# Kernel tuning notes

Hardware: AMD Instinct MI355X
Metric: run time of the kernel (lower is better)

## Reference

```python
import jax, jax.numpy as jnp
import numpy as np

N_EMBD = 1024
NUM_HEADS = 16
HEAD_DIM = N_EMBD // NUM_HEADS
B, N = 4, 1024
EPS = 1e-5


def _ln(x, w, b):
    mu = jnp.mean(x, axis=-1, keepdims=True)
    var = jnp.var(x, axis=-1, keepdims=True)
    return (x - mu) * jax.lax.rsqrt(var + EPS) * w + b


def setup_inputs() -> dict:
    key = jax.random.key(0)
    ks = jax.random.split(key, 12)
    s = 0.02
    d, dff = N_EMBD, 4 * N_EMBD
    return {
        "x": jax.random.normal(ks[0], (B, N, d), dtype=jnp.float32),
        "ln1_w": jnp.ones((d,), jnp.float32),
        "ln1_b": jnp.zeros((d,), jnp.float32),
        "Wq": jax.random.normal(ks[1], (d, d), jnp.float32) * s,
        "bq": jnp.zeros((d,), jnp.float32),
        "Wk": jax.random.normal(ks[2], (d, d), jnp.float32) * s,
        "bk": jnp.zeros((d,), jnp.float32),
        "Wv": jax.random.normal(ks[3], (d, d), jnp.float32) * s,
        "bv": jnp.zeros((d,), jnp.float32),
        "Wo": jax.random.normal(ks[4], (d, d), jnp.float32) * s,
        "bo": jnp.zeros((d,), jnp.float32),
        "ln2_w": jnp.ones((d,), jnp.float32),
        "ln2_b": jnp.zeros((d,), jnp.float32),
        "Wfc": jax.random.normal(ks[5], (d, dff), jnp.float32) * s,
        "bfc": jnp.zeros((dff,), jnp.float32),
        "Wproj": jax.random.normal(ks[6], (dff, d), jnp.float32) * s,
        "bproj": jnp.zeros((d,), jnp.float32),
    }


def reference(x, ln1_w, ln1_b, Wq, bq, Wk, bk, Wv, bv, Wo, bo,
              ln2_w, ln2_b, Wfc, bfc, Wproj, bproj):
    # --- attention sublayer ---
    h = _ln(x, ln1_w, ln1_b)  # [B,N,D]
    q = (h @ Wq + bq).reshape(B, N, NUM_HEADS, HEAD_DIM).transpose(0, 2, 1, 3)
    k = (h @ Wk + bk).reshape(B, N, NUM_HEADS, HEAD_DIM).transpose(0, 2, 1, 3)
    v = (h @ Wv + bv).reshape(B, N, NUM_HEADS, HEAD_DIM).transpose(0, 2, 1, 3)
    scale = 1.0 / np.sqrt(HEAD_DIM).astype(np.float32)
    attn = jax.nn.softmax(jnp.einsum("bhqd,bhkd->bhqk", q, k) * scale, axis=-1)
    o = jnp.einsum("bhqk,bhkd->bhqd", attn, v)  # [B,H,N,Dh]
    o = o.transpose(0, 2, 1, 3).reshape(B, N, N_EMBD)
    x = x + (o @ Wo + bo)
    # --- MLP sublayer (exact GELU, matching torch nn.GELU default) ---
    h2 = _ln(x, ln2_w, ln2_b)
    h2 = jax.nn.gelu(h2 @ Wfc + bfc, approximate=False)
    x = x + (h2 @ Wproj + bproj)
    return x
```

## Files before the change

### kernel.cpp

```cpp
#include <hip/hip_runtime.h>
#include <hip/hip_bf16.h>

typedef unsigned short u16;
typedef u16 u16x8 __attribute__((ext_vector_type(8)));
typedef u16 u16x4 __attribute__((ext_vector_type(4)));
typedef __bf16 bf16x8 __attribute__((ext_vector_type(8)));
typedef float f32x4 __attribute__((ext_vector_type(4)));

__device__ __forceinline__ u16 f2bf(float f) {
  union { __hip_bfloat16 h; u16 u; } cv;
  cv.h = __float2bfloat16(f);
  return cv.u;
}
__device__ __forceinline__ float bf2f(u16 u) {
  union { unsigned u; float f; } c;
  c.u = ((unsigned)u) << 16;
  return c.f;
}

__device__ __forceinline__ void glds16(const void* g, void* l) {
  __builtin_amdgcn_global_load_lds(
      (const __attribute__((address_space(1))) unsigned int*)g,
      (__attribute__((address_space(3))) unsigned int*)l, 16, 0, 0);
}

__global__ __launch_bounds__(256) void transpose_bf16(const float* __restrict__ W,
                                                      u16* __restrict__ Wt,
                                                      int K, int N) {
  __shared__ float tile[32][33];
  int tx = threadIdx.x, ty = threadIdx.y;
  int n0 = blockIdx.x * 32, k0 = blockIdx.y * 32;
#pragma unroll
  for (int j = 0; j < 4; ++j)
    tile[ty + j * 8][tx] = W[(size_t)(k0 + ty + j * 8) * N + n0 + tx];
  __syncthreads();
#pragma unroll
  for (int j = 0; j < 4; ++j)
    Wt[(size_t)(n0 + ty + j * 8) * K + k0 + tx] = f2bf(tile[tx][ty + j * 8]);
}

__global__ __launch_bounds__(256) void ln_kernel(const float* __restrict__ x,
                                                 const float* __restrict__ w,
                                                 const float* __restrict__ b,
                                                 u16* __restrict__ out) {
  int row = blockIdx.x, t = threadIdx.x;
  const float* xr = x + (size_t)row * 1024;
  float4 v = *reinterpret_cast<const float4*>(xr + t * 4);
  float s = v.x + v.y + v.z + v.w;
  float s2 = v.x * v.x + v.y * v.y + v.z * v.z + v.w * v.w;
#pragma unroll
  for (int m = 1; m < 64; m <<= 1) {
    s += __shfl_xor(s, m, 64);
    s2 += __shfl_xor(s2, m, 64);
  }
  __shared__ float red[8];
  if ((t & 63) == 0) { red[t >> 6] = s; red[(t >> 6) + 4] = s2; }
  __syncthreads();
  s = red[0] + red[1] + red[2] + red[3];
  s2 = red[4] + red[5] + red[6] + red[7];
  float mu = s * (1.f / 1024.f);
  float var = s2 * (1.f / 1024.f) - mu * mu;
  float rs = rsqrtf(var + 1e-5f);
  float4 wv = *reinterpret_cast<const float4*>(w + t * 4);
  float4 bv = *reinterpret_cast<const float4*>(b + t * 4);
  u16x4 o;
  o.x = f2bf((v.x - mu) * rs * wv.x + bv.x);
  o.y = f2bf((v.y - mu) * rs * wv.y + bv.y);
  o.z = f2bf((v.z - mu) * rs * wv.z + bv.z);
  o.w = f2bf((v.w - mu) * rs * wv.w + bv.w);
  *reinterpret_cast<u16x4*>(out + (size_t)row * 1024 + t * 4) = o;
}

template <int MODE>
__global__ __launch_bounds__(512, 2) void gemm256(
    const u16* __restrict__ A, const u16* __restrict__ Bt,
    const float* __restrict__ b0, const float* __restrict__ b1,
    const float* __restrict__ b2,
    u16* __restrict__ o0, u16* __restrict__ o1, u16* __restrict__ o2,
    int Kfull, int KL, int MT, int NT, float qscale) {
  __shared__ u16 lds[2][2][2][256 * 32];
  const int tid = threadIdx.x;
  const int lane = tid & 63, w = tid >> 6;
  const int wm = w >> 2, wn = w & 3;
  const int l15 = lane & 15, l4 = lane >> 4;
  const int skey = (l15 >> 1) & 3;

  const int nwg = gridDim.x;
  int wg = (int)blockIdx.x;
  wg = (wg & 7) * (nwg >> 3) + (wg >> 3);
  const int mt = wg % MT;
  int rest = wg / MT;
  const int nt = rest % NT;
  const int zt = rest / NT;

  const int row0 = mt * 256, col0 = nt * 256;
  const int kbase = zt * KL;
  const int nkt = KL >> 6;

  auto stage = [&](int buf, int op, int ks, int kt) {
    const u16* src = op ? Bt : A;
    const int base = op ? col0 : row0;
    const int kb = kbase + (kt << 6) + (ks << 5);
    u16* dst = &lds[buf][op][ks][0];
#pragma unroll
    for (int i = 0; i < 2; ++i) {
      int c = i * 512 + tid;
      int r = c >> 2, ch = c & 3;
      int sch = ch ^ ((r >> 1) & 3);
      glds16(src + (size_t)(base + r) * Kfull + kb + sch * 8, dst + c * 8);
    }
  };
  auto rdA = [&](int buf, int ks, int m) -> bf16x8 {
    int row = wm * 128 + m * 16 + l15;
    return *reinterpret_cast<const bf16x8*>(&lds[buf][0][ks][row * 32 + ((l4 ^ skey) << 3)]);
  };
  auto rdB = [&](int buf, int ks, int n) -> bf16x8 {
    int row = wn * 64 + n * 16 + l15;
    return *reinterpret_cast<const bf16x8*>(&lds[buf][1][ks][row * 32 + ((l4 ^ skey) << 3)]);
  };

  f32x4 acc[8][4];
#pragma unroll
  for (int m = 0; m < 8; ++m)
#pragma unroll
    for (int n = 0; n < 4; ++n) acc[m][n] = (f32x4){0.f, 0.f, 0.f, 0.f};

  stage(0, 0, 0, 0);
  stage(0, 0, 1, 0);
  stage(0, 1, 0, 0);
  stage(0, 1, 1, 0);
  asm volatile("s_waitcnt vmcnt(2)" ::: "memory");
  __builtin_amdgcn_s_barrier();

  bf16x8 af[8];
  for (int t = 0; t < nkt; ++t) {
    const int cur = t & 1, nxt = cur ^ 1;
    const bool pf = (t + 1 < nkt);
    {
#pragma unroll
      for (int m = 0; m < 8; ++m) af[m] = rdA(cur, 0, m);
      bf16x8 bq0 = rdB(cur, 0, 0), bq1 = rdB(cur, 0, 1);
      if (pf) stage(nxt, 0, 0, t + 1);
      __builtin_amdgcn_s_barrier();
      __builtin_amdgcn_s_setprio(1);
#pragma unroll
      for (int m = 0; m < 8; ++m) {
        acc[m][0] = __builtin_amdgcn_mfma_f32_16x16x32_bf16(af[m], bq0, acc[m][0], 0, 0, 0);
        acc[m][1] = __builtin_amdgcn_mfma_f32_16x16x32_bf16(af[m], bq1, acc[m][1], 0, 0, 0);
      }
      __builtin_amdgcn_s_setprio(0);
      __builtin_amdgcn_s_barrier();
    }
    {
      bf16x8 bq2 = rdB(cur, 0, 2), bq3 = rdB(cur, 0, 3);
      if (pf) {
        stage(nxt, 0, 1, t + 1);
        asm volatile("s_waitcnt vmcnt(4)" ::: "memory");
      } else {
        asm volatile("s_waitcnt vmcnt(0)" ::: "memory");
      }
      __builtin_amdgcn_s_barrier();
      __builtin_amdgcn_s_setprio(1);
#pragma unroll
      for (int m = 0; m < 8; ++m) {
        acc[m][2] = __builtin_amdgcn_mfma_f32_16x16x32_bf16(af[m], bq2, acc[m][2], 0, 0, 0);
        acc[m][3] = __builtin_amdgcn_mfma_f32_16x16x32_bf16(af[m], bq3, acc[m][3], 0, 0, 0);
      }
      __builtin_amdgcn_s_setprio(0);
      __builtin_amdgcn_s_barrier();
    }
    {
#pragma unroll
      for (int m = 0; m < 8; ++m) af[m] = rdA(cur, 1, m);
      bf16x8 bq0 = rdB(cur, 1, 0), bq1 = rdB(cur, 1, 1);
      if (pf) stage(nxt, 1, 0, t + 1);
      __builtin_amdgcn_s_barrier();
      __builtin_amdgcn_s_setprio(1);
#pragma unroll
      for (int m = 0; m < 8; ++m) {
        acc[m][0] = __builtin_amdgcn_mfma_f32_16x16x32_bf16(af[m], bq0, acc[m][0], 0, 0, 0);
        acc[m][1] = __builtin_amdgcn_mfma_f32_16x16x32_bf16(af[m], bq1, acc[m][1], 0, 0, 0);
      }
      __builtin_amdgcn_s_setprio(0);
      __builtin_amdgcn_s_barrier();
    }
    {
      bf16x8 bq2 = rdB(cur, 1, 2), bq3 = rdB(cur, 1, 3);
      if (pf) stage(nxt, 1, 1, t + 1);
      asm volatile("s_waitcnt vmcnt(2)" ::: "memory");
      __builtin_amdgcn_s_barrier();
      __builtin_amdgcn_s_setprio(1);
#pragma unroll
      for (int m = 0; m < 8; ++m) {
        acc[m][2] = __builtin_amdgcn_mfma_f32_16x16x32_bf16(af[m], bq2, acc[m][2], 0, 0, 0);
        acc[m][3] = __builtin_amdgcn_mfma_f32_16x16x32_bf16(af[m], bq3, acc[m][3], 0, 0, 0);
      }
      __builtin_amdgcn_s_setprio(0);
      __builtin_amdgcn_s_barrier();
    }
  }

  if constexpr (MODE == 0) {
    const int which = nt >> 2;
    const int bidx = mt >> 2;
#pragma unroll
    for (int m = 0; m < 8; ++m)
#pragma unroll
      for (int n = 0; n < 4; ++n) {
        int colc = (col0 & 1023) + wn * 64 + n * 16 + l15;
        int hh = colc >> 6, d = colc & 63;
        int nb = (row0 & 1023) + wm * 128 + m * 16 + l4 * 4;
        if (which == 2) {
          u16x4 pk;
#pragma unroll
          for (int r = 0; r < 4; ++r) pk[r] = f2bf(acc[m][n][r] + b2[colc]);
          *reinterpret_cast<u16x4*>(o2 + (((size_t)(bidx * 16 + hh) * 64 + d) * 1024 + nb)) = pk;
        } else {
          const float* bb = (which == 0) ? b0 : b1;
          u16* dst = (which == 0) ? o0 : o1;
          float sc = (which == 0) ? qscale : 1.0f;
#pragma unroll
          for (int r = 0; r < 4; ++r)
            dst[((size_t)(bidx * 16 + hh) * 1024 + nb + r) * 64 + d] =
                f2bf((acc[m][n][r] + bb[colc]) * sc);
        }
      }
  } else if constexpr (MODE == 2) {
    const int N = NT * 256;
#pragma unroll
    for (int m = 0; m < 8; ++m)
#pragma unroll
      for (int n = 0; n < 4; ++n)
#pragma unroll
        for (int r = 0; r < 4; ++r) {
          int row = row0 + wm * 128 + m * 16 + l4 * 4 + r;
          int col = col0 + wn * 64 + n * 16 + l15;
          float val = acc[m][n][r] + b0[col];
          float g = 0.5f * val * (1.0f + erff(val * 0.70710678118f));
          o0[(size_t)row * N + col] = f2bf(g);
        }
  } else {
    const int M = MT * 256, N = NT * 256;
    u16* base = o0 + (size_t)zt * M * N;
#pragma unroll
    for (int m = 0; m < 8; ++m)
#pragma unroll
      for (int n = 0; n < 4; ++n)
#pragma unroll
        for (int r = 0; r < 4; ++r) {
          int row = row0 + wm * 128 + m * 16 + l4 * 4 + r;
          int col = col0 + wn * 64 + n * 16 + l15;
          base[(size_t)row * N + col] = f2bf(acc[m][n][r]);
        }
  }
}

__global__ __launch_bounds__(256) void proj_reduce(const u16* __restrict__ parts,
                                                   const float* __restrict__ bias,
                                                   const float* __restrict__ res,
                                                   float* __restrict__ out) {
  size_t i = ((size_t)blockIdx.x * 256 + threadIdx.x) * 8;
  int col = (int)(i & 1023);
  float s[8];
  float4 r0 = *reinterpret_cast<const float4*>(res + i);
  float4 r1 = *reinterpret_cast<const float4*>(res + i + 4);
  s[0] = r0.x; s[1] = r0.y; s[2] = r0.z; s[3] = r0.w;
  s[4] = r1.x; s[5] = r1.y; s[6] = r1.z; s[7] = r1.w;
#pragma unroll
  for (int j = 0; j < 8; ++j) s[j] += bias[col + j];
#pragma unroll
  for (int sp = 0; sp < 4; ++sp) {
    u16x8 pv = *reinterpret_cast<const u16x8*>(parts + (size_t)sp * 4096 * 1024 + i);
#pragma unroll
    for (int j = 0; j < 8; ++j) s[j] += bf2f(pv[j]);
  }
  float4 o0 = {s[0], s[1], s[2], s[3]};
  float4 o1 = {s[4], s[5], s[6], s[7]};
  *reinterpret_cast<float4*>(out + i) = o0;
  *reinterpret_cast<float4*>(out + i + 4) = o1;
}

template <int MODE, int TN>
__global__ __launch_bounds__(256) void gemm_k(
    const u16* __restrict__ A, const u16* __restrict__ Bt,
    const float* __restrict__ b0, const float* __restrict__ res,
    float* __restrict__ of, int M, int N, int K) {
  constexpr int WHALF = TN / 2;
  constexpr int NF = TN / 32;
  __shared__ u16 As[2][128 * 32];
  __shared__ u16 Bs[2][TN * 32];
  const int tid = threadIdx.x;
  const int lane = tid & 63, w = tid >> 6;
  const int wr = w >> 1, wc = w & 1;
  const int l15 = lane & 15, l4 = lane >> 4;
  const int row0 = blockIdx.x * 128, col0 = blockIdx.y * TN;
  f32x4 acc[4][NF];
#pragma unroll
  for (int m = 0; m < 4; ++m)
#pragma unroll
    for (int n = 0; n < NF; ++n) acc[m][n] = (f32x4){0.f, 0.f, 0.f, 0.f};

  auto stage = [&](int buf, int k0) {
#pragma unroll
    for (int i = 0; i < 2; ++i) {
      int c = i * 256 + tid;
      glds16(A + (size_t)(row0 + (c >> 2)) * K + k0 + (c & 3) * 8, &As[buf][c * 8]);
    }
    if constexpr (TN == 128) {
#pragma unroll
      for (int i = 0; i < 2; ++i) {
        int c = i * 256 + tid;
        glds16(Bt + (size_t)(col0 + (c >> 2)) * K + k0 + (c & 3) * 8, &Bs[buf][c * 8]);
      }
    } else {
      int c = tid;
      glds16(Bt + (size_t)(col0 + (c >> 2)) * K + k0 + (c & 3) * 8, &Bs[buf][c * 8]);
    }
  };

  stage(0, 0);
  __syncthreads();
  const int nk = K >> 5;
  for (int t = 0; t < nk; ++t) {
    int cur = t & 1;
    if (t + 1 < nk) stage(cur ^ 1, (t + 1) << 5);
    bf16x8 af[4], bfr[NF];
#pragma unroll
    for (int m = 0; m < 4; ++m)
      af[m] = *reinterpret_cast<const bf16x8*>(&As[cur][(wr * 64 + m * 16 + l15) * 32 + l4 * 8]);
#pragma unroll
    for (int n = 0; n < NF; ++n)
      bfr[n] = *reinterpret_cast<const bf16x8*>(&Bs[cur][(wc * WHALF + n * 16 + l15) * 32 + l4 * 8]);
#pragma unroll
    for (int m = 0; m < 4; ++m)
#pragma unroll
      for (int n = 0; n < NF; ++n)
        acc[m][n] = __builtin_amdgcn_mfma_f32_16x16x32_bf16(af[m], bfr[n], acc[m][n], 0, 0, 0);
    __syncthreads();
  }

#pragma unroll
  for (int m = 0; m < 4; ++m)
#pragma unroll
    for (int n = 0; n < NF; ++n)
#pragma unroll
      for (int r = 0; r < 4; ++r) {
        int row = row0 + wr * 64 + m * 16 + l4 * 4 + r;
        int col = col0 + wc * WHALF + n * 16 + l15;
        of[(size_t)row * N + col] = acc[m][n][r] + b0[col] + res[(size_t)row * N + col];
      }
}

__global__ __launch_bounds__(256) void attn_kernel(const u16* __restrict__ q,
                                                   const u16* __restrict__ k,
                                                   const u16* __restrict__ vt,
                                                   u16* __restrict__ o) {
  const int bh = blockIdx.x, qb = blockIdx.y;
  const int b = bh >> 4, h = bh & 15;
  __shared__ u16 Ks[2][4096];
  __shared__ u16 Vt[2][4096];
  __shared__ u16 Ps[4][1024];
  const int tid = threadIdx.x, lane = tid & 63, w = tid >> 6;
  const int l15 = lane & 15, l4 = lane >> 4;
  const int sw = l15 & 7;
  const u16* kbase = k + (size_t)bh * 65536;
  const u16* vtbase = vt + (size_t)bh * 65536;

  const u16* qrow = q + ((size_t)bh * 1024 + qb * 64 + w * 16 + l15) * 64;
  bf16x8 qf0 = *reinterpret_cast<const bf16x8*>(qrow + l4 * 8);
  bf16x8 qf1 = *reinterpret_cast<const bf16x8*>(qrow + 32 + l4 * 8);

  auto stageKV = [&](int buf, int kv0) {
#pragma unroll
    for (int i = 0; i < 2; ++i) {
      int c = i * 256 + tid, r = c >> 3, sl = (c & 7) ^ (r & 7);
      glds16(kbase + (size_t)(kv0 + r) * 64 + sl * 8, &Ks[buf][c * 8]);
    }
#pragma unroll
    for (int i = 0; i < 2; ++i) {
      int c = i * 256 + tid, r = c >> 3, sl = (c & 7) ^ (r & 7);
      glds16(vtbase + (size_t)r * 1024 + kv0 + sl * 8, &Vt[buf][c * 8]);
    }
  };

  f32x4 oacc[4];
#pragma unroll
  for (int n = 0; n < 4; ++n) oacc[n] = (f32x4){0.f, 0.f, 0.f, 0.f};
  float mrow[4], lrow[4];
#pragma unroll
  for (int r = 0; r < 4; ++r) { mrow[r] = -3.0e38f; lrow[r] = 0.f; }

  stageKV(0, 0);
  __syncthreads();

  for (int kv0 = 0; kv0 < 1024; kv0 += 64) {
    int cur = (kv0 >> 6) & 1;
    if (kv0 + 64 < 1024) stageKV(cur ^ 1, kv0 + 64);

    f32x4 st[4];
#pragma unroll
    for (int t = 0; t < 4; ++t) {
      int row = t * 16 + l15;
      f32x4 s = (f32x4){0.f, 0.f, 0.f, 0.f};
      bf16x8 kf0 = *reinterpret_cast<const bf16x8*>(&Ks[cur][row * 64 + ((l4 ^ sw) << 3)]);
      s = __builtin_amdgcn_mfma_f32_16x16x32_bf16(qf0, kf0, s, 0, 0, 0);
      bf16x8 kf1 = *reinterpret_cast<const bf16x8*>(&Ks[cur][row * 64 + (((4 + l4) ^ sw) << 3)]);
      s = __builtin_amdgcn_mfma_f32_16x16x32_bf16(qf1, kf1, s, 0, 0, 0);
      st[t] = s;
    }

    float tmax[4];
#pragma unroll
    for (int r = 0; r < 4; ++r)
      tmax[r] = fmaxf(fmaxf(st[0][r], st[1][r]), fmaxf(st[2][r], st[3][r]));
#pragma unroll
    for (int md = 1; md < 16; md <<= 1)
#pragma unroll
      for (int r = 0; r < 4; ++r) tmax[r] = fmaxf(tmax[r], __shfl_xor(tmax[r], md, 64));
    float pr[4][4], alpha[4], rsum[4];
#pragma unroll
    for (int r = 0; r < 4; ++r) {
      float mnew = fmaxf(mrow[r], tmax[r]);
      alpha[r] = exp2f(mrow[r] - mnew);
      mrow[r] = mnew;
#pragma unroll
      for (int t = 0; t < 4; ++t) pr[t][r] = exp2f(st[t][r] - mnew);
      rsum[r] = (pr[0][r] + pr[1][r]) + (pr[2][r] + pr[3][r]);
    }
#pragma unroll
    for (int md = 1; md < 16; md <<= 1)
#pragma unroll
      for (int r = 0; r < 4; ++r) rsum[r] += __shfl_xor(rsum[r], md, 64);
#pragma unroll
    for (int r = 0; r < 4; ++r) lrow[r] = lrow[r] * alpha[r] + rsum[r];
#pragma unroll
    for (int n = 0; n < 4; ++n)
#pragma unroll
      for (int r = 0; r < 4; ++r) oacc[n][r] *= alpha[r];

#pragma unroll
    for (int t = 0; t < 4; ++t)
#pragma unroll
      for (int r = 0; r < 4; ++r) {
        int qq = l4 * 4 + r, kv = t * 16 + l15;
        Ps[w][qq * 64 + ((((kv >> 3) ^ (qq & 7)) << 3) | (kv & 7))] = f2bf(pr[t][r]);
      }

#pragma unroll
    for (int c2 = 0; c2 < 2; ++c2) {
      bf16x8 pf = *reinterpret_cast<const bf16x8*>(
          &Ps[w][l15 * 64 + ((((c2 << 2) + l4) ^ sw) << 3)]);
#pragma unroll
      for (int n = 0; n < 4; ++n) {
        bf16x8 vf = *reinterpret_cast<const bf16x8*>(
            &Vt[cur][(n * 16 + l15) * 64 + ((((c2 << 2) + l4) ^ sw) << 3)]);
        oacc[n] = __builtin_amdgcn_mfma_f32_16x16x32_bf16(pf, vf, oacc[n], 0, 0, 0);
      }
    }
    __syncthreads();
  }

  float invl[4];
#pragma unroll
  for (int r = 0; r < 4; ++r) invl[r] = 1.0f / lrow[r];
#pragma unroll
  for (int n = 0; n < 4; ++n)
#pragma unroll
    for (int r = 0; r < 4; ++r) {
      int nr = qb * 64 + w * 16 + l4 * 4 + r;
      int dc = n * 16 + l15;
      o[((size_t)(b * 1024 + nr)) * 1024 + h * 64 + dc] = f2bf(oacc[n][r] * invl[r]);
    }
}

extern "C" void kernel_launch(void* const* d_in, const int* in_sizes, int n_in,
                              void* d_out, int out_size, void* d_ws, size_t ws_size,
                              hipStream_t stream) {
  (void)in_sizes; (void)n_in; (void)out_size; (void)ws_size;
  const float* x     = (const float*)d_in[0];
  const float* ln1w  = (const float*)d_in[1];
  const float* ln1b  = (const float*)d_in[2];
  const float* Wq    = (const float*)d_in[3];
  const float* bq    = (const float*)d_in[4];
  const float* Wk    = (const float*)d_in[5];
  const float* bk    = (const float*)d_in[6];
  const float* Wv    = (const float*)d_in[7];
  const float* bv    = (const float*)d_in[8];
  const float* Wo    = (const float*)d_in[9];
  const float* bo    = (const float*)d_in[10];
  const float* ln2w  = (const float*)d_in[11];
  const float* ln2b  = (const float*)d_in[12];
  const float* Wfc   = (const float*)d_in[13];
  const float* bfc   = (const float*)d_in[14];
  const float* Wproj = (const float*)d_in[15];
  const float* bproj = (const float*)d_in[16];
  float* out = (float*)d_out;

  char* p = (char*)d_ws;
  u16* hb     = (u16*)p; p += (size_t)4096 * 1024 * 2;
  u16* WqkvT  = (u16*)p; p += (size_t)3072 * 1024 * 2;
  u16* WoT    = (u16*)p; p += (size_t)1024 * 1024 * 2;
  u16* WfcT   = (u16*)p; p += (size_t)4096 * 1024 * 2;
  u16* WprojT = (u16*)p; p += (size_t)1024 * 4096 * 2;
  u16* qb_    = (u16*)p; p += (size_t)4096 * 1024 * 2;
  u16* kb_    = (u16*)p; p += (size_t)4096 * 1024 * 2;
  u16* vt_    = (u16*)p; p += (size_t)4096 * 1024 * 2;
  u16* ob_    = (u16*)p; p += (size_t)4096 * 1024 * 2;
  float* x1   = (float*)p; p += (size_t)4096 * 1024 * 4;
  u16* h2     = (u16*)p; p += (size_t)4096 * 1024 * 2;
  u16* ffnb   = (u16*)p; p += (size_t)4096 * 4096 * 2;

  const float qscale = 0.125f * 1.44269504089f;

  dim3 tb(32, 8);
  transpose_bf16<<<dim3(32, 32), tb, 0, stream>>>(Wq, WqkvT, 1024, 1024);
  transpose_bf16<<<dim3(32, 32), tb, 0, stream>>>(Wk, WqkvT + (size_t)1024 * 1024, 1024, 1024);
  transpose_bf16<<<dim3(32, 32), tb, 0, stream>>>(Wv, WqkvT + (size_t)2048 * 1024, 1024, 1024);
  transpose_bf16<<<dim3(32, 32), tb, 0, stream>>>(Wo, WoT, 1024, 1024);
  transpose_bf16<<<dim3(128, 32), tb, 0, stream>>>(Wfc, WfcT, 1024, 4096);
  transpose_bf16<<<dim3(32, 128), tb, 0, stream>>>(Wproj, WprojT, 4096, 1024);

  ln_kernel<<<4096, 256, 0, stream>>>(x, ln1w, ln1b, hb);

  gemm256<0><<<192, 512, 0, stream>>>(hb, WqkvT, bq, bk, bv,
                                      qb_, kb_, vt_, 1024, 1024, 16, 12, qscale);

  attn_kernel<<<dim3(64, 16), 256, 0, stream>>>(qb_, kb_, vt_, ob_);

  gemm_k<1, 64><<<dim3(32, 16), 256, 0, stream>>>(ob_, WoT, bo, x, x1, 4096, 1024, 1024);

  ln_kernel<<<4096, 256, 0, stream>>>(x1, ln2w, ln2b, h2);

  gemm256<2><<<256, 512, 0, stream>>>(h2, WfcT, bfc, nullptr, nullptr,
                                      ffnb, nullptr, nullptr, 1024, 1024, 16, 16, 1.f);

  gemm256<3><<<256, 512, 0, stream>>>(ffnb, WprojT, nullptr, nullptr, nullptr,
                                      qb_, nullptr, nullptr, 4096, 1024, 16, 4, 1.f);
  proj_reduce<<<2048, 256, 0, stream>>>(qb_, bproj, x1, out);
}
```

Baseline: 376.2 us.

## Merge weight transposes, split-K Wo GEMM, and restructure attention softmax

Four small weight transposes are merged into one launch via a z-grid dimension. The Wo projection now uses the 256-tile split-K gemm256 kernel writing bf16 partials into four reused buffers, followed by a reduce kernel that adds bias and residual, replacing the smaller gemm_k kernel. The attention kernel swaps MFMA operand order so each lane owns one query row, which cuts the cross-lane shuffles for max and sum. It also skips rescaling of the running output unless the max grows by more than a threshold, and writes P and the output as packed 4-wide stores. Partial sums are now stored in bf16 for the Wo path, which adds rounding error and extra memory traffic for the reduce.

Measured after the change: 358.8 us. 1.05x faster.

```diff
diff --git a/kernel.cpp b/kernel.cpp
--- a/kernel.cpp
+++ b/kernel.cpp
@@ -37,6 +37,27 @@
 #pragma unroll
   for (int j = 0; j < 4; ++j)
     Wt[(size_t)(n0 + ty + j * 8) * K + k0 + tx] = f2bf(tile[tx][ty + j * 8]);
+}
+
+__global__ __launch_bounds__(256) void transpose4(const float* __restrict__ W0,
+                                                  const float* __restrict__ W1,
+                                                  const float* __restrict__ W2,
+                                                  const float* __restrict__ W3,
+                                                  u16* __restrict__ T0, u16* __restrict__ T1,
+                                                  u16* __restrict__ T2, u16* __restrict__ T3) {
+  __shared__ float tile[32][33];
+  int z = blockIdx.z;
+  const float* W = (z == 0) ? W0 : (z == 1) ? W1 : (z == 2) ? W2 : W3;
+  u16* T = (z == 0) ? T0 : (z == 1) ? T1 : (z == 2) ? T2 : T3;
+  int tx = threadIdx.x, ty = threadIdx.y;
+  int n0 = blockIdx.x * 32, k0 = blockIdx.y * 32;
+#pragma unroll
+  for (int j = 0; j < 4; ++j)
+    tile[ty + j * 8][tx] = W[(size_t)(k0 + ty + j * 8) * 1024 + n0 + tx];
+  __syncthreads();
+#pragma unroll
+  for (int j = 0; j < 4; ++j)
+    T[(size_t)(n0 + ty + j * 8) * 1024 + k0 + tx] = f2bf(tile[tx][ty + j * 8]);
 }
 
 __global__ __launch_bounds__(256) void ln_kernel(const float* __restrict__ x,
@@ -77,6 +98,7 @@
     const float* __restrict__ b0, const float* __restrict__ b1,
     const float* __restrict__ b2,
     u16* __restrict__ o0, u16* __restrict__ o1, u16* __restrict__ o2,
+    u16* __restrict__ o3,
     int Kfull, int KL, int MT, int NT, float qscale) {
   __shared__ u16 lds[2][2][2][256 * 32];
   const int tid = threadIdx.x;
@@ -240,8 +262,8 @@
           o0[(size_t)row * N + col] = f2bf(g);
         }
   } else {
-    const int M = MT * 256, N = NT * 256;
-    u16* base = o0 + (size_t)zt * M * N;
+    const int N = NT * 256;
+    u16* base = (zt == 0) ? o0 : (zt == 1) ? o1 : (zt == 2) ? o2 : o3;
 #pragma unroll
     for (int m = 0; m < 8; ++m)
 #pragma unroll
@@ -255,10 +277,13 @@
   }
 }
 
-__global__ __launch_bounds__(256) void proj_reduce(const u16* __restrict__ parts,
-                                                   const float* __restrict__ bias,
-                                                   const float* __restrict__ res,
-                                                   float* __restrict__ out) {
+__global__ __launch_bounds__(256) void reduce4(const u16* __restrict__ p0,
+                                               const u16* __restrict__ p1,
+                                               const u16* __restrict__ p2,
+                                               const u16* __restrict__ p3,
+                                               const float* __restrict__ bias,
+                                               const float* __restrict__ res,
+                                               float* __restrict__ out) {
   size_t i = ((size_t)blockIdx.x * 256 + threadIdx.x) * 8;
   int col = (int)(i & 1023);
   float s[8];
@@ -268,9 +293,10 @@
   s[4] = r1.x; s[5] = r1.y; s[6] = r1.z; s[7] = r1.w;
 #pragma unroll
   for (int j = 0; j < 8; ++j) s[j] += bias[col + j];
+  const u16* ps[4] = {p0, p1, p2, p3};
 #pragma unroll
   for (int sp = 0; sp < 4; ++sp) {
-    u16x8 pv = *reinterpret_cast<const u16x8*>(parts + (size_t)sp * 4096 * 1024 + i);
+    u16x8 pv = *reinterpret_cast<const u16x8*>(ps[sp] + i);
 #pragma unroll
     for (int j = 0; j < 8; ++j) s[j] += bf2f(pv[j]);
   }
@@ -278,77 +304,6 @@
   float4 o1 = {s[4], s[5], s[6], s[7]};
   *reinterpret_cast<float4*>(out + i) = o0;
   *reinterpret_cast<float4*>(out + i + 4) = o1;
-}
-
-template <int MODE, int TN>
-__global__ __launch_bounds__(256) void gemm_k(
-    const u16* __restrict__ A, const u16* __restrict__ Bt,
-    const float* __restrict__ b0, const float* __restrict__ res,
-    float* __restrict__ of, int M, int N, int K) {
-  constexpr int WHALF = TN / 2;
-  constexpr int NF = TN / 32;
-  __shared__ u16 As[2][128 * 32];
-  __shared__ u16 Bs[2][TN * 32];
-  const int tid = threadIdx.x;
-  const int lane = tid & 63, w = tid >> 6;
-  const int wr = w >> 1, wc = w & 1;
-  const int l15 = lane & 15, l4 = lane >> 4;
-  const int row0 = blockIdx.x * 128, col0 = blockIdx.y * TN;
-  f32x4 acc[4][NF];
-#pragma unroll
-  for (int m = 0; m < 4; ++m)
-#pragma unroll
-    for (int n = 0; n < NF; ++n) acc[m][n] = (f32x4){0.f, 0.f, 0.f, 0.f};
-
-  auto stage = [&](int buf, int k0) {
-#pragma unroll
-    for (int i = 0; i < 2; ++i) {
-      int c = i * 256 + tid;
-      glds16(A + (size_t)(row0 + (c >> 2)) * K + k0 + (c & 3) * 8, &As[buf][c * 8]);
-    }
-    if constexpr (TN == 128) {
-#pragma unroll
-      for (int i = 0; i < 2; ++i) {
-        int c = i * 256 + tid;
-        glds16(Bt + (size_t)(col0 + (c >> 2)) * K + k0 + (c & 3) * 8, &Bs[buf][c * 8]);
-      }
-    } else {
-      int c = tid;
-      glds16(Bt + (size_t)(col0 + (c >> 2)) * K + k0 + (c & 3) * 8, &Bs[buf][c * 8]);
-    }
-  };
-
-  stage(0, 0);
-  __syncthreads();
-  const int nk = K >> 5;
-  for (int t = 0; t < nk; ++t) {
-    int cur = t & 1;
-    if (t + 1 < nk) stage(cur ^ 1, (t + 1) << 5);
-    bf16x8 af[4], bfr[NF];
-#pragma unroll
-    for (int m = 0; m < 4; ++m)
-      af[m] = *reinterpret_cast<const bf16x8*>(&As[cur][(wr * 64 + m * 16 + l15) * 32 + l4 * 8]);
-#pragma unroll
-    for (int n = 0; n < NF; ++n)
-      bfr[n] = *reinterpret_cast<const bf16x8*>(&Bs[cur][(wc * WHALF + n * 16 + l15) * 32 + l4 * 8]);
-#pragma unroll
-    for (int m = 0; m < 4; ++m)
-#pragma unroll
-      for (int n = 0; n < NF; ++n)
-        acc[m][n] = __builtin_amdgcn_mfma_f32_16x16x32_bf16(af[m], bfr[n], acc[m][n], 0, 0, 0);
-    __syncthreads();
-  }
-
-#pragma unroll
-  for (int m = 0; m < 4; ++m)
-#pragma unroll
-    for (int n = 0; n < NF; ++n)
-#pragma unroll
-      for (int r = 0; r < 4; ++r) {
-        int row = row0 + wr * 64 + m * 16 + l4 * 4 + r;
-        int col = col0 + wc * WHALF + n * 16 + l15;
-        of[(size_t)row * N + col] = acc[m][n][r] + b0[col] + res[(size_t)row * N + col];
-      }
 }
 
 __global__ __launch_bounds__(256) void attn_kernel(const u16* __restrict__ q,
@@ -386,9 +341,7 @@
   f32x4 oacc[4];
 #pragma unroll
   for (int n = 0; n < 4; ++n) oacc[n] = (f32x4){0.f, 0.f, 0.f, 0.f};
-  float mrow[4], lrow[4];
-#pragma unroll
-  for (int r = 0; r < 4; ++r) { mrow[r] = -3.0e38f; lrow[r] = 0.f; }
+  float mrow = -3.0e38f, lrow = 0.f;
 
   stageKV(0, 0);
   __syncthreads();
@@ -403,74 +356,75 @@
       int row = t * 16 + l15;
       f32x4 s = (f32x4){0.f, 0.f, 0.f, 0.f};
       bf16x8 kf0 = *reinterpret_cast<const bf16x8*>(&Ks[cur][row * 64 + ((l4 ^ sw) << 3)]);
-      s = __builtin_amdgcn_mfma_f32_16x16x32_bf16(qf0, kf0, s, 0, 0, 0);
+      s = __builtin_amdgcn_mfma_f32_16x16x32_bf16(kf0, qf0, s, 0, 0, 0);
       bf16x8 kf1 = *reinterpret_cast<const bf16x8*>(&Ks[cur][row * 64 + (((4 + l4) ^ sw) << 3)]);
-      s = __builtin_amdgcn_mfma_f32_16x16x32_bf16(qf1, kf1, s, 0, 0, 0);
+      s = __builtin_amdgcn_mfma_f32_16x16x32_bf16(kf1, qf1, s, 0, 0, 0);
       st[t] = s;
     }
 
-    float tmax[4];
-#pragma unroll
-    for (int r = 0; r < 4; ++r)
-      tmax[r] = fmaxf(fmaxf(st[0][r], st[1][r]), fmaxf(st[2][r], st[3][r]));
-#pragma unroll
-    for (int md = 1; md < 16; md <<= 1)
-#pragma unroll
-      for (int r = 0; r < 4; ++r) tmax[r] = fmaxf(tmax[r], __shfl_xor(tmax[r], md, 64));
-    float pr[4][4], alpha[4], rsum[4];
-#pragma unroll
-    for (int r = 0; r < 4; ++r) {
-      float mnew = fmaxf(mrow[r], tmax[r]);
-      alpha[r] = exp2f(mrow[r] - mnew);
-      mrow[r] = mnew;
-#pragma unroll
-      for (int t = 0; t < 4; ++t) pr[t][r] = exp2f(st[t][r] - mnew);
-      rsum[r] = (pr[0][r] + pr[1][r]) + (pr[2][r] + pr[3][r]);
-    }
-#pragma unroll
-    for (int md = 1; md < 16; md <<= 1)
-#pragma unroll
-      for (int r = 0; r < 4; ++r) rsum[r] += __shfl_xor(rsum[r], md, 64);
-#pragma unroll
-    for (int r = 0; r < 4; ++r) lrow[r] = lrow[r] * alpha[r] + rsum[r];
-#pragma unroll
-    for (int n = 0; n < 4; ++n)
-#pragma unroll
-      for (int r = 0; r < 4; ++r) oacc[n][r] *= alpha[r];
-
+    float tm = st[0][0];
 #pragma unroll
     for (int t = 0; t < 4; ++t)
 #pragma unroll
+      for (int r = 0; r < 4; ++r) tm = fmaxf(tm, st[t][r]);
+    tm = fmaxf(tm, __shfl_xor(tm, 16, 64));
+    tm = fmaxf(tm, __shfl_xor(tm, 32, 64));
+    if (!__all(tm - mrow <= 8.f)) {
+      float mnew = fmaxf(mrow, tm);
+      float al = exp2f(mrow - mnew);
+      lrow *= al;
+#pragma unroll
+      for (int n = 0; n < 4; ++n)
+#pragma unroll
+        for (int r = 0; r < 4; ++r) oacc[n][r] *= al;
+      mrow = mnew;
+    }
+    float pr[4][4];
+    float ps = 0.f;
+#pragma unroll
+    for (int t = 0; t < 4; ++t)
+#pragma unroll
       for (int r = 0; r < 4; ++r) {
-        int qq = l4 * 4 + r, kv = t * 16 + l15;
-        Ps[w][qq * 64 + ((((kv >> 3) ^ (qq & 7)) << 3) | (kv & 7))] = f2bf(pr[t][r]);
-      }
+        pr[t][r] = exp2f(st[t][r] - mrow);
+        ps += pr[t][r];
+      }
+    ps += __shfl_xor(ps, 16, 64);
+    ps += __shfl_xor(ps, 32, 64);
+    lrow += ps;
+
+#pragma unroll
+    for (int t = 0; t < 4; ++t) {
+      u16x4 pk;
+#pragma unroll
+      for (int r = 0; r < 4; ++r) pk[r] = f2bf(pr[t][r]);
+      int swch = ((t << 1) | (l4 >> 1)) ^ sw;
+      *reinterpret_cast<u16x4*>(&Ps[w][l15 * 64 + swch * 8 + (l4 & 1) * 4]) = pk;
+    }
 
 #pragma unroll
     for (int c2 = 0; c2 < 2; ++c2) {
       bf16x8 pf = *reinterpret_cast<const bf16x8*>(
-          &Ps[w][l15 * 64 + ((((c2 << 2) + l4) ^ sw) << 3)]);
+          &Ps[w][l15 * 64 + ((((c2 << 2) | l4) ^ sw) << 3)]);
 #pragma unroll
       for (int n = 0; n < 4; ++n) {
         bf16x8 vf = *reinterpret_cast<const bf16x8*>(
-            &Vt[cur][(n * 16 + l15) * 64 + ((((c2 << 2) + l4) ^ sw) << 3)]);
-        oacc[n] = __builtin_amdgcn_mfma_f32_16x16x32_bf16(pf, vf, oacc[n], 0, 0, 0);
+            &Vt[cur][(n * 16 + l15) * 64 + ((((c2 << 2) | l4) ^ sw) << 3)]);
+        oacc[n] = __builtin_amdgcn_mfma_f32_16x16x32_bf16(vf, pf, oacc[n], 0, 0, 0);
       }
     }
     __syncthreads();
   }
 
-  float invl[4];
-#pragma unroll
-  for (int r = 0; r < 4; ++r) invl[r] = 1.0f / lrow[r];
-#pragma unroll
-  for (int n = 0; n < 4; ++n)
-#pragma unroll
-    for (int r = 0; r < 4; ++r) {
-      int nr = qb * 64 + w * 16 + l4 * 4 + r;
-      int dc = n * 16 + l15;
-      o[((size_t)(b * 1024 + nr)) * 1024 + h * 64 + dc] = f2bf(oacc[n][r] * invl[r]);
-    }
+  float inv = 1.0f / lrow;
+  int nr = qb * 64 + w * 16 + l15;
+#pragma unroll
+  for (int n = 0; n < 4; ++n) {
+    u16x4 pk;
+#pragma unroll
+    for (int r = 0; r < 4; ++r) pk[r] = f2bf(oacc[n][r] * inv);
+    *reinterpret_cast<u16x4*>(
+        o + ((size_t)(b * 1024 + nr)) * 1024 + h * 64 + n * 16 + l4 * 4) = pk;
+  }
 }
 
 extern "C" void kernel_launch(void* const* d_in, const int* in_sizes, int n_in,
@@ -513,28 +467,29 @@
   const float qscale = 0.125f * 1.44269504089f;
 
   dim3 tb(32, 8);
-  transpose_bf16<<<dim3(32, 32), tb, 0, stream>>>(Wq, WqkvT, 1024, 1024);
-  transpose_bf16<<<dim3(32, 32), tb, 0, stream>>>(Wk, WqkvT + (size_t)1024 * 1024, 1024, 1024);
-  transpose_bf16<<<dim3(32, 32), tb, 0, stream>>>(Wv, WqkvT + (size_t)2048 * 1024, 1024, 1024);
-  transpose_bf16<<<dim3(32, 32), tb, 0, stream>>>(Wo, WoT, 1024, 1024);
+  transpose4<<<dim3(32, 32, 4), tb, 0, stream>>>(Wq, Wk, Wv, Wo,
+                                                 WqkvT, WqkvT + (size_t)1024 * 1024,
+                                                 WqkvT + (size_t)2048 * 1024, WoT);
   transpose_bf16<<<dim3(128, 32), tb, 0, stream>>>(Wfc, WfcT, 1024, 4096);
   transpose_bf16<<<dim3(32, 128), tb, 0, stream>>>(Wproj, WprojT, 4096, 1024);
 
   ln_kernel<<<4096, 256, 0, stream>>>(x, ln1w, ln1b, hb);
 
   gemm256<0><<<192, 512, 0, stream>>>(hb, WqkvT, bq, bk, bv,
-                                      qb_, kb_, vt_, 1024, 1024, 16, 12, qscale);
+                                      qb_, kb_, vt_, nullptr, 1024, 1024, 16, 12, qscale);
 
   attn_kernel<<<dim3(64, 16), 256, 0, stream>>>(qb_, kb_, vt_, ob_);
 
-  gemm_k<1, 64><<<dim3(32, 16), 256, 0, stream>>>(ob_, WoT, bo, x, x1, 4096, 1024, 1024);
+  gemm256<3><<<256, 512, 0, stream>>>(ob_, WoT, nullptr, nullptr, nullptr,
+                                      qb_, kb_, vt_, h2, 1024, 256, 16, 4, 1.f);
+  reduce4<<<2048, 256, 0, stream>>>(qb_, kb_, vt_, h2, bo, x, x1);
 
   ln_kernel<<<4096, 256, 0, stream>>>(x1, ln2w, ln2b, h2);
 
   gemm256<2><<<256, 512, 0, stream>>>(h2, WfcT, bfc, nullptr, nullptr,
-                                      ffnb, nullptr, nullptr, 1024, 1024, 16, 16, 1.f);
+                                      ffnb, nullptr, nullptr, nullptr, 1024, 1024, 16, 16, 1.f);
 
   gemm256<3><<<256, 512, 0, stream>>>(ffnb, WprojT, nullptr, nullptr, nullptr,
-                                      qb_, nullptr, nullptr, 4096, 1024, 16, 4, 1.f);
-  proj_reduce<<<2048, 256, 0, stream>>>(qb_, bproj, x1, out);
-}
+                                      qb_, kb_, vt_, ob_, 4096, 1024, 16, 4, 1.f);
+  reduce4<<<2048, 256, 0, stream>>>(qb_, kb_, vt_, ob_, bproj, x1, out);
+}
```
